# Optimization experiments

Measured on AMD Instinct MI355X. Metric: run time of the kernel, lower is better.

The kernel has to match this reference:

```python
import jax, jax.numpy as jnp
import numpy as np

B, T, D = 8, 512, 64

def setup_inputs() -> dict:
    key = jax.random.key(0)
    kx, kw, kb = jax.random.split(key, 3)
    x = jax.random.normal(kx, (B, T, D), dtype=jnp.float32)
    W = jax.random.normal(kw, (D, D), dtype=jnp.float32) / np.sqrt(D)
    b = jax.random.normal(kb, (D,), dtype=jnp.float32) * 0.01
    return {"x": x, "W": W, "b": b}

def reference(x, W, b):
    # v = Linear(x): (B,T,D)
    v = jnp.einsum('btd,ed->bte', x, W) + b
    # pairwise diff: (B,T,T,D); softmax over feature dim D
    diff = x[:, :, None, :] - x[:, None, :, :]
    K = jax.nn.softmax(-(diff * diff), axis=-1)
    # out[b,i,j] = sum_d K[b,i,j,d] * v[b,i,d]  -> (B,T,T)
    out = jnp.einsum('bijd,bid->bij', K, v)
    return out
```

## Files before the change

### kernel.cpp

```cpp
#include <hip/hip_runtime.h>

#define BB 8
#define TT 512
#define DD 64
#define S_SCALE 1.2011224087864498f

typedef float v2f __attribute__((ext_vector_type(2)));
typedef _Float16 h8 __attribute__((ext_vector_type(8)));
typedef _Float16 v2h __attribute__((ext_vector_type(2)));

static __device__ __forceinline__ float fast_exp2(float v) {
#if __has_builtin(__builtin_amdgcn_exp2f)
    return __builtin_amdgcn_exp2f(v);
#else
    return exp2f(v);
#endif
}
static __device__ __forceinline__ float fast_rcp(float v) {
#if __has_builtin(__builtin_amdgcn_rcpf)
    return __builtin_amdgcn_rcpf(v);
#else
    return 1.0f / v;
#endif
}
static __device__ __forceinline__ v2f pk_fma(v2f a, v2f b, v2f c) {
#if __has_builtin(__builtin_elementwise_fma)
    return __builtin_elementwise_fma(a, b, c);
#else
    return a * b + c;
#endif
}
static __device__ __forceinline__ v2f cvt2(v2h h) {
    return __builtin_convertvector(h, v2f);
}

__global__ __launch_bounds__(256) void rbf_pre(
    const float* __restrict__ x, const float* __restrict__ W,
    const float* __restrict__ bias,
    _Float16* __restrict__ xh, _Float16* __restrict__ vh,
    float* __restrict__ vv)
{
    const int t = threadIdx.x;
    const int w = t >> 6, l = t & 63;
    const int row = blockIdx.x * 4 + w;
    const float* xr = x + (size_t)row * DD;
    const float* wr = W + (size_t)l * DD;
    float acc = bias[l];
    #pragma unroll
    for (int d = 0; d < DD; d += 4) {
        float4 xv = *(const float4*)(xr + d);
        float4 wv = *(const float4*)(wr + d);
        acc = fmaf(xv.x, wv.x, acc); acc = fmaf(xv.y, wv.y, acc);
        acc = fmaf(xv.z, wv.z, acc); acc = fmaf(xv.w, wv.w, acc);
    }
    xh[(size_t)row * DD + l] = (_Float16)(xr[l] * S_SCALE);
    vh[(size_t)row * DD + l] = (_Float16)acc;
    vv[(size_t)row * DD + l] = acc;
}

template <bool MIRROR>
static __device__ __forceinline__ void tile_compute(
    const _Float16* xls, const _Float16* vls,
    const float* xis, const float* vis,
    float* __restrict__ orow0, float* cbuf, int l, int wau)
{
    v2f nr[2][2], nc[2][2], dn[2];
    #pragma unroll
    for (int r = 0; r < 2; ++r) {
        nr[r][0] = (v2f){0.f, 0.f}; nr[r][1] = (v2f){0.f, 0.f};
        nc[r][0] = (v2f){0.f, 0.f}; nc[r][1] = (v2f){0.f, 0.f};
        dn[r]    = (v2f){0.f, 0.f};
    }

    #pragma unroll
    for (int c = 0; c < 8; ++c) {
        h8 xjh = *(const h8*)(xls + l * 72 + c * 8);
        h8 vjh = *(const h8*)(vls + l * 72 + c * 8);
        const v2h* xjp = (const v2h*)&xjh;
        const v2h* vjp = (const v2h*)&vjh;
        #pragma unroll
        for (int r = 0; r < 2; ++r) {
            const v2f* xi2 = (const v2f*)(xis + (wau * 2 + r) * DD + c * 8);
            const v2f* vi2 = (const v2f*)(vis + (wau * 2 + r) * DD + c * 8);
            #pragma unroll
            for (int q = 0; q < 4; ++q) {
                v2f u = xi2[q] - cvt2(xjp[q]);
                u *= u;
                v2f e = {fast_exp2(-u.x), fast_exp2(-u.y)};
                nr[r][q & 1] = pk_fma(e, vi2[q], nr[r][q & 1]);
                if (MIRROR) nc[r][q & 1] = pk_fma(e, cvt2(vjp[q]), nc[r][q & 1]);
                dn[r] += e;
            }
        }
    }

    #pragma unroll
    for (int r = 0; r < 2; ++r) {
        float rd = fast_rcp(dn[r].x + dn[r].y);
        v2f sr = nr[r][0] + nr[r][1];
        orow0[(size_t)r * TT + l] = (sr.x + sr.y) * rd;
        if (MIRROR) {
            v2f sc = nc[r][0] + nc[r][1];
            cbuf[l * 12 + wau * 2 + r] = (sc.x + sc.y) * rd;
        }
    }
}

__global__ __launch_bounds__(256, 8) void rbf_sym(
    const float* __restrict__ x,
    const _Float16* __restrict__ xh, const _Float16* __restrict__ vh,
    const float* __restrict__ vv, float* __restrict__ out)
{
    const int bid = blockIdx.x;
    const int b = bid / 288;
    int idx = bid - b * 288;
    int ti, jt, isA;
    if (idx < 64) { jt = idx >> 3; ti = 8 * jt + (idx & 7); isA = 0; }
    else {
        int k = idx - 64, t = 1;
        while (k >= 8 * t) { k -= 8 * t; ++t; }
        jt = t; ti = k; isA = 1;
    }
    const int i0 = ti * 8, j0 = jt * 64;

    const int tid = threadIdx.x;
    const int w = tid >> 6, l = tid & 63;
    const int wau = __builtin_amdgcn_readfirstlane(w);

    __shared__ __align__(16) _Float16 xls[64 * 72];
    __shared__ __align__(16) _Float16 vls[64 * 72];
    __shared__ __align__(16) float xis[8 * DD];
    __shared__ __align__(16) float vis[8 * DD];
    __shared__ float cbuf[64 * 12];

    {
        const uint4* xsrc = (const uint4*)(xh + ((size_t)b * TT + j0) * DD);
        const uint4* vsrc = (const uint4*)(vh + ((size_t)b * TT + j0) * DD);
        #pragma unroll
        for (int u = 0; u < 2; ++u) {
            int g = u * 256 + tid;
            int r = g >> 3, c = g & 7;
            *(uint4*)(xls + r * 72 + c * 8) = xsrc[g];
            *(uint4*)(vls + r * 72 + c * 8) = vsrc[g];
        }
        int g = tid & 127;
        int r = g >> 4, c4 = (g & 15) * 4;
        if (tid < 128) {
            float4 v = *(const float4*)(x + ((size_t)(b * TT + i0 + r)) * DD + c4);
            v.x *= S_SCALE; v.y *= S_SCALE; v.z *= S_SCALE; v.w *= S_SCALE;
            *(float4*)(xis + r * DD + c4) = v;
        } else {
            *(float4*)(vis + r * DD + c4) =
                *(const float4*)(vv + ((size_t)(b * TT + i0 + r)) * DD + c4);
        }
    }
    __syncthreads();

    float* outb  = out + (size_t)b * TT * TT;
    float* orow0 = outb + (size_t)(i0 + wau * 2) * TT + j0;

    if (isA) tile_compute<true >(xls, vls, xis, vis, orow0, cbuf, l, wau);
    else     tile_compute<false>(xls, vls, xis, vis, orow0, cbuf, l, wau);

    __syncthreads();
    if (isA && tid < 128) {
        int j = tid >> 1, qf = (tid & 1) * 4;
        float4 cv = *(const float4*)(cbuf + j * 12 + qf);
        *(float4*)(outb + (size_t)(j0 + j) * TT + i0 + qf) = cv;
    }
}

extern "C" void kernel_launch(void* const* d_in, const int* in_sizes, int n_in,
                              void* d_out, int out_size, void* d_ws, size_t ws_size,
                              hipStream_t stream) {
    const float* x    = (const float*)d_in[0];
    const float* W    = (const float*)d_in[1];
    const float* bias = (const float*)d_in[2];
    float* out        = (float*)d_out;

    _Float16* xh = (_Float16*)d_ws;
    _Float16* vh = (_Float16*)((char*)d_ws + (1 << 19));
    float*    vv = (float*)((char*)d_ws + (1 << 20));

    rbf_pre<<<BB * TT / 4, 256, 0, stream>>>(x, W, bias, xh, vh, vv);
    rbf_sym<<<BB * 288, 256, 0, stream>>>(x, xh, vh, vv, out);
}
```

Baseline: 85.14 us.

## Use fp32 j-tiles and 16-row i-tiles with 512-thread blocks

New measurement: 85.93 us. About the same (+0.9%).

```diff
diff --git a/kernel.cpp b/kernel.cpp
--- a/kernel.cpp
+++ b/kernel.cpp
@@ -6,8 +6,6 @@
 #define S_SCALE 1.2011224087864498f
 
 typedef float v2f __attribute__((ext_vector_type(2)));
-typedef _Float16 h8 __attribute__((ext_vector_type(8)));
-typedef _Float16 v2h __attribute__((ext_vector_type(2)));
 
 static __device__ __forceinline__ float fast_exp2(float v) {
 #if __has_builtin(__builtin_amdgcn_exp2f)
@@ -30,15 +28,11 @@
     return a * b + c;
 #endif
 }
-static __device__ __forceinline__ v2f cvt2(v2h h) {
-    return __builtin_convertvector(h, v2f);
-}
 
 __global__ __launch_bounds__(256) void rbf_pre(
     const float* __restrict__ x, const float* __restrict__ W,
     const float* __restrict__ bias,
-    _Float16* __restrict__ xh, _Float16* __restrict__ vh,
-    float* __restrict__ vv)
+    float* __restrict__ xs, float* __restrict__ vv)
 {
     const int t = threadIdx.x;
     const int w = t >> 6, l = t & 63;
@@ -53,106 +47,103 @@
         acc = fmaf(xv.x, wv.x, acc); acc = fmaf(xv.y, wv.y, acc);
         acc = fmaf(xv.z, wv.z, acc); acc = fmaf(xv.w, wv.w, acc);
     }
-    xh[(size_t)row * DD + l] = (_Float16)(xr[l] * S_SCALE);
-    vh[(size_t)row * DD + l] = (_Float16)acc;
+    xs[(size_t)row * DD + l] = xr[l] * S_SCALE;
     vv[(size_t)row * DD + l] = acc;
 }
 
 template <bool MIRROR>
 static __device__ __forceinline__ void tile_compute(
-    const _Float16* xls, const _Float16* vls,
+    const float* xls, const float* vls,
     const float* xis, const float* vis,
     float* __restrict__ orow0, float* cbuf, int l, int wau)
 {
-    v2f nr[2][2], nc[2][2], dn[2];
+    v2f nr[2][2], nc[2][2], dn[2][2];
     #pragma unroll
     for (int r = 0; r < 2; ++r) {
         nr[r][0] = (v2f){0.f, 0.f}; nr[r][1] = (v2f){0.f, 0.f};
         nc[r][0] = (v2f){0.f, 0.f}; nc[r][1] = (v2f){0.f, 0.f};
-        dn[r]    = (v2f){0.f, 0.f};
+        dn[r][0] = (v2f){0.f, 0.f}; dn[r][1] = (v2f){0.f, 0.f};
     }
 
-    #pragma unroll
-    for (int c = 0; c < 8; ++c) {
-        h8 xjh = *(const h8*)(xls + l * 72 + c * 8);
-        h8 vjh = *(const h8*)(vls + l * 72 + c * 8);
-        const v2h* xjp = (const v2h*)&xjh;
-        const v2h* vjp = (const v2h*)&vjh;
+    #pragma unroll 4
+    for (int c = 0; c < 16; ++c) {
+        float4 xj4 = *(const float4*)(xls + l * 68 + c * 4);
+        float4 vj4 = *(const float4*)(vls + l * 68 + c * 4);
+        const v2f* xjp = (const v2f*)&xj4;
+        const v2f* vjp = (const v2f*)&vj4;
         #pragma unroll
         for (int r = 0; r < 2; ++r) {
-            const v2f* xi2 = (const v2f*)(xis + (wau * 2 + r) * DD + c * 8);
-            const v2f* vi2 = (const v2f*)(vis + (wau * 2 + r) * DD + c * 8);
+            const v2f* xi2 = (const v2f*)(xis + (wau * 2 + r) * DD + c * 4);
+            const v2f* vi2 = (const v2f*)(vis + (wau * 2 + r) * DD + c * 4);
             #pragma unroll
-            for (int q = 0; q < 4; ++q) {
-                v2f u = xi2[q] - cvt2(xjp[q]);
+            for (int q = 0; q < 2; ++q) {
+                v2f u = xi2[q] - xjp[q];
                 u *= u;
                 v2f e = {fast_exp2(-u.x), fast_exp2(-u.y)};
-                nr[r][q & 1] = pk_fma(e, vi2[q], nr[r][q & 1]);
-                if (MIRROR) nc[r][q & 1] = pk_fma(e, cvt2(vjp[q]), nc[r][q & 1]);
-                dn[r] += e;
+                nr[r][q] = pk_fma(e, vi2[q], nr[r][q]);
+                if (MIRROR) nc[r][q] = pk_fma(e, vjp[q], nc[r][q]);
+                dn[r][q] += e;
             }
         }
     }
 
     #pragma unroll
     for (int r = 0; r < 2; ++r) {
-        float rd = fast_rcp(dn[r].x + dn[r].y);
+        v2f d2 = dn[r][0] + dn[r][1];
+        float rd = fast_rcp(d2.x + d2.y);
         v2f sr = nr[r][0] + nr[r][1];
         orow0[(size_t)r * TT + l] = (sr.x + sr.y) * rd;
         if (MIRROR) {
             v2f sc = nc[r][0] + nc[r][1];
-            cbuf[l * 12 + wau * 2 + r] = (sc.x + sc.y) * rd;
+            cbuf[l * 20 + wau * 2 + r] = (sc.x + sc.y) * rd;
         }
     }
 }
 
-__global__ __launch_bounds__(256, 8) void rbf_sym(
-    const float* __restrict__ x,
-    const _Float16* __restrict__ xh, const _Float16* __restrict__ vh,
-    const float* __restrict__ vv, float* __restrict__ out)
+__global__ __launch_bounds__(512, 4) void rbf_sym(
+    const float* __restrict__ xs, const float* __restrict__ vv,
+    float* __restrict__ out)
 {
     const int bid = blockIdx.x;
-    const int b = bid / 288;
-    int idx = bid - b * 288;
+    const int b = bid / 144;
+    int idx = bid - b * 144;
     int ti, jt, isA;
-    if (idx < 64) { jt = idx >> 3; ti = 8 * jt + (idx & 7); isA = 0; }
+    if (idx < 32) { jt = idx >> 2; ti = 4 * jt + (idx & 3); isA = 0; }
     else {
-        int k = idx - 64, t = 1;
-        while (k >= 8 * t) { k -= 8 * t; ++t; }
+        int k = idx - 32, t = 1;
+        while (k >= 4 * t) { k -= 4 * t; ++t; }
         jt = t; ti = k; isA = 1;
     }
-    const int i0 = ti * 8, j0 = jt * 64;
+    const int i0 = ti * 16, j0 = jt * 64;
 
     const int tid = threadIdx.x;
     const int w = tid >> 6, l = tid & 63;
     const int wau = __builtin_amdgcn_readfirstlane(w);
 
-    __shared__ __align__(16) _Float16 xls[64 * 72];
-    __shared__ __align__(16) _Float16 vls[64 * 72];
-    __shared__ __align__(16) float xis[8 * DD];
-    __shared__ __align__(16) float vis[8 * DD];
-    __shared__ float cbuf[64 * 12];
+    __shared__ __align__(16) float xls[64 * 68];
+    __shared__ __align__(16) float vls[64 * 68];
+    __shared__ __align__(16) float xis[16 * DD];
+    __shared__ __align__(16) float vis[16 * DD];
+    __shared__ __align__(16) float cbuf[64 * 20];
 
     {
-        const uint4* xsrc = (const uint4*)(xh + ((size_t)b * TT + j0) * DD);
-        const uint4* vsrc = (const uint4*)(vh + ((size_t)b * TT + j0) * DD);
+        const float4* xsrc = (const float4*)(xs + ((size_t)b * TT + j0) * DD);
+        const float4* vsrc = (const float4*)(vv + ((size_t)b * TT + j0) * DD);
         #pragma unroll
-        for (int u = 0; u < 2; ++u) {
-            int g = u * 256 + tid;
-            int r = g >> 3, c = g & 7;
-            *(uint4*)(xls + r * 72 + c * 8) = xsrc[g];
-            *(uint4*)(vls + r * 72 + c * 8) = vsrc[g];
+        for (int k = 0; k < 2; ++k) {
+            int g = k * 512 + tid;
+            int r = g >> 4, c4 = (g & 15) * 4;
+            *(float4*)(xls + r * 68 + c4) = xsrc[g];
+            *(float4*)(vls + r * 68 + c4) = vsrc[g];
         }
-        int g = tid & 127;
+        int g = tid & 255;
         int r = g >> 4, c4 = (g & 15) * 4;
-        if (tid < 128) {
-            float4 v = *(const float4*)(x + ((size_t)(b * TT + i0 + r)) * DD + c4);
-            v.x *= S_SCALE; v.y *= S_SCALE; v.z *= S_SCALE; v.w *= S_SCALE;
-            *(float4*)(xis + r * DD + c4) = v;
-        } else {
+        if (tid < 256)
+            *(float4*)(xis + r * DD + c4) =
+                *(const float4*)(xs + ((size_t)(b * TT + i0 + r)) * DD + c4);
+        else
             *(float4*)(vis + r * DD + c4) =
                 *(const float4*)(vv + ((size_t)(b * TT + i0 + r)) * DD + c4);
-        }
     }
     __syncthreads();
 
@@ -162,11 +153,13 @@
     if (isA) tile_compute<true >(xls, vls, xis, vis, orow0, cbuf, l, wau);
     else     tile_compute<false>(xls, vls, xis, vis, orow0, cbuf, l, wau);
 
-    __syncthreads();
-    if (isA && tid < 128) {
-        int j = tid >> 1, qf = (tid & 1) * 4;
-        float4 cv = *(const float4*)(cbuf + j * 12 + qf);
-        *(float4*)(outb + (size_t)(j0 + j) * TT + i0 + qf) = cv;
+    if (isA) {
+        __syncthreads();
+        if (tid < 256) {
+            int j = tid >> 2, qf = (tid & 3) * 4;
+            float4 cv = *(const float4*)(cbuf + j * 20 + qf);
+            *(float4*)(outb + (size_t)(j0 + j) * TT + i0 + qf) = cv;
+        }
     }
 }
 
@@ -178,10 +171,9 @@
     const float* bias = (const float*)d_in[2];
     float* out        = (float*)d_out;
 
-    _Float16* xh = (_Float16*)d_ws;
-    _Float16* vh = (_Float16*)((char*)d_ws + (1 << 19));
-    float*    vv = (float*)((char*)d_ws + (1 << 20));
+    float* xs = (float*)d_ws;
+    float* vv = (float*)((char*)d_ws + (1 << 20));
 
-    rbf_pre<<<BB * TT / 4, 256, 0, stream>>>(x, W, bias, xh, vh, vv);
-    rbf_sym<<<BB * 288, 256, 0, stream>>>(x, xh, vh, vv, out);
+    rbf_pre<<<BB * TT / 4, 256, 0, stream>>>(x, W, bias, xs, vv);
+    rbf_sym<<<BB * 144, 512, 0, stream>>>(xs, vv, out);
 }
```
